# Optimization experiments

Measured on AMD Instinct MI355X. Metric: run time of the kernel, lower is better.

The kernel has to match this reference:

```python
import jax, jax.numpy as jnp
import numpy as np

N_NODES = 50000
N_EDGES = 1600000
IN_FEATS = 128
ENC_H = 20
DEC_H = 64


def setup_inputs() -> dict:
    key = jax.random.key(0)
    ks = jax.random.split(key, 14)
    inp = {}
    inp["x"] = jax.random.normal(ks[0], (N_NODES, IN_FEATS), dtype=jnp.float32)
    inp["edge_index"] = jax.random.randint(ks[1], (2, N_EDGES), 0, N_NODES, dtype=jnp.int64)
    inp["node_id"] = 0
    inp["noise_normal"] = jax.random.normal(ks[2], (N_EDGES, ENC_H), dtype=jnp.float32)
    inp["noise_u"] = jax.random.uniform(ks[3], (N_EDGES, 1), dtype=jnp.float32)
    # parameters (glorot-ish init)
    def lin(k, fan_in, fan_out):
        s = 1.0 / np.sqrt(fan_in)
        return jax.random.uniform(k, (fan_in, fan_out), jnp.float32, -s, s)
    inp["W_gc"] = lin(ks[4], IN_FEATS, ENC_H)
    inp["b_gc"] = jnp.zeros((ENC_H,), jnp.float32)
    inp["W_mu"] = lin(ks[5], 3 * ENC_H, ENC_H)
    inp["b_mu"] = jnp.zeros((ENC_H,), jnp.float32)
    inp["W_var"] = lin(ks[6], 3 * ENC_H, ENC_H)
    inp["b_var"] = jnp.zeros((ENC_H,), jnp.float32)
    inp["W_d1"] = lin(ks[7], ENC_H, DEC_H)
    inp["b_d1"] = jnp.zeros((DEC_H,), jnp.float32)
    inp["W_d2"] = lin(ks[8], DEC_H, 1)
    inp["b_d2"] = jnp.zeros((1,), jnp.float32)
    return inp


def _gcn_conv(x, edge_index, W, b):
    """PyG-style GCNConv: add self-loops, symmetric D^-1/2 (A+I) D^-1/2 norm."""
    n = x.shape[0]
    sl = jnp.arange(n, dtype=edge_index.dtype)
    row = jnp.concatenate([edge_index[0], sl])  # source
    col = jnp.concatenate([edge_index[1], sl])  # target
    xw = x @ W  # [N, H]
    deg = jax.ops.segment_sum(jnp.ones_like(col, dtype=xw.dtype), col, num_segments=n)
    dinv = jnp.where(deg > 0, jax.lax.rsqrt(deg), 0.0)
    norm = dinv[row] * dinv[col]  # [E+N]
    out = jax.ops.segment_sum(xw[row] * norm[:, None], col, num_segments=n)
    return out + b


def reference(x, edge_index, node_id, noise_normal, noise_u,
              W_gc, b_gc, W_mu, b_mu, W_var, b_var, W_d1, b_d1, W_d2, b_d2):
    # GCN encoder
    x1 = jax.nn.relu(_gcn_conv(x, edge_index, W_gc, b_gc))  # [N, H]
    # per-edge concat: [src_embed | dst_embed | node_id_embed]
    rows, cols = edge_index[0], edge_index[1]
    node_embed = jnp.broadcast_to(x1[node_id][None, :], (rows.shape[0], x1.shape[1]))
    x2 = jnp.concatenate([x1[rows], x1[cols], node_embed], axis=1)  # [E, 3H]
    # variational heads + reparameterization
    mu = x2 @ W_mu + b_mu
    sigma = jnp.exp(x2 @ W_var + b_var)
    z = mu + sigma * noise_normal  # [E, H]
    # decoder MLP
    h = jax.nn.relu(z @ W_d1 + b_d1)
    sampling_weights = jax.nn.relu(h @ W_d2 + b_d2)  # [E, 1]
    # gumbel-sigmoid sample (training=True, bias=0.0 -> bias'=1e-4, temperature=1.0)
    bias = 0.0001
    eps = (bias - (1.0 - bias)) * noise_u + (1.0 - bias)
    gate = jnp.log(eps) - jnp.log(1.0 - eps) + sampling_weights
    return jax.nn.sigmoid(gate)
```

## Files before the change

kernel.cpp:

```cpp
#include <hip/hip_runtime.h>

#define NFEAT 128
#define H 20
#define DH 64
#define SCAN_T 1024
#define BE 64
#define CAP 96

typedef __attribute__((ext_vector_type(8))) short short8;
typedef __attribute__((ext_vector_type(4))) float f32x4;

__device__ __forceinline__ unsigned short f2bf(float f) {
    union { float f; unsigned u; } v; v.f = f;
    unsigned r = v.u + 0x7fff + ((v.u >> 16) & 1);
    return (unsigned short)(r >> 16);
}
__device__ __forceinline__ unsigned pk2(unsigned short a, unsigned short b) {
    return (unsigned)a | ((unsigned)b << 16);
}

template <int CTRL>
__device__ __forceinline__ float dpp_add(float x) {
    int y = __builtin_amdgcn_update_dpp(0, __float_as_int(x), CTRL, 0xF, 0xF, true);
    return x + __int_as_float(y);
}
__device__ __forceinline__ float sum16(float x) {
    x = dpp_add<0xB1>(x);
    x = dpp_add<0x4E>(x);
    x = dpp_add<0x124>(x);
    x = dpp_add<0x128>(x);
    return x;
}

__global__ __launch_bounds__(256) void k_prep(const float* __restrict__ Wmu, const float* __restrict__ Wvar,
                                              const float* __restrict__ Wd1,
                                              const float* __restrict__ bmu, const float* __restrict__ bvar,
                                              unsigned short* __restrict__ Bh, unsigned short* __restrict__ Bd1,
                                              float* __restrict__ bcat, int* __restrict__ deg, int N) {
    int t = blockIdx.x * blockDim.x + threadIdx.x;
    if (t < N) deg[t] = 0;
    if (t < 512) {
        int f = t >> 6, l = t & 63;
        int tile = f >> 1, s = f & 1;
        int col = (tile & 1) * 16 + (l & 15);
        const float* W = (tile < 2) ? Wmu : Wvar;
#pragma unroll
        for (int j = 0; j < 8; j++) {
            int k = s * 32 + (l >> 4) * 8 + j;
            float v = (k < 3 * H && col < H) ? W[k * H + col] : 0.f;
            Bh[(size_t)f * 512 + l * 8 + j] = f2bf(v);
        }
    } else if (t < 768) {
        int f = (t - 512) >> 6, l = t & 63;
        int n = f * 16 + (l & 15);
#pragma unroll
        for (int j = 0; j < 8; j++) {
            int k = (l >> 4) * 8 + j;
            float v = (k < H) ? Wd1[k * DH + n] : 0.f;
            Bd1[(size_t)f * 512 + l * 8 + j] = f2bf(v);
        }
    } else if (t < 808) {
        int c = t - 768;
        bcat[c] = (c < H) ? bmu[c] : bvar[c - H];
    }
}

__global__ __launch_bounds__(256) void k_bucket_slots(const int* __restrict__ rows, const int* __restrict__ cols,
                                                      int* __restrict__ deg, unsigned short* __restrict__ slots, int E) {
    int e = blockIdx.x * blockDim.x + threadIdx.x;
    if (e >= E) return;
    int c = __builtin_nontemporal_load(cols + e);
    int r = __builtin_nontemporal_load(rows + e);
    int pos = atomicAdd(&deg[c], 1);
    if (pos < CAP) slots[(size_t)c * CAP + pos] = (unsigned short)r;
}

__global__ __launch_bounds__(256) void k_deg(const int* __restrict__ cols, int* __restrict__ deg, int E) {
    int t = blockIdx.x * blockDim.x + threadIdx.x;
    if (t < E) atomicAdd(&deg[cols[t]], 1);
}

__global__ __launch_bounds__(SCAN_T) void k_scan(const int* __restrict__ deg, int* __restrict__ offsets,
                                                 int* __restrict__ cursor, int N) {
    __shared__ int sums[SCAN_T];
    int t = threadIdx.x;
    int chunk = (N + SCAN_T - 1) / SCAN_T;
    int beg = t * chunk;
    int end = min(beg + chunk, N);
    int s = 0;
    for (int i = beg; i < end; i++) s += deg[i];
    sums[t] = s;
    __syncthreads();
    for (int off = 1; off < SCAN_T; off <<= 1) {
        int v = (t >= off) ? sums[t - off] : 0;
        __syncthreads();
        sums[t] += v;
        __syncthreads();
    }
    int run = (t == 0) ? 0 : sums[t - 1];
    for (int i = beg; i < end; i++) {
        offsets[i] = run;
        cursor[i] = run;
        run += deg[i];
    }
    if (t == SCAN_T - 1) offsets[N] = sums[SCAN_T - 1];
}

__global__ __launch_bounds__(256) void k_bucket_csr(const int* __restrict__ rows, const int* __restrict__ cols,
                                                    int* __restrict__ cursor, int* __restrict__ srcs, int E) {
    int e = blockIdx.x * blockDim.x + threadIdx.x;
    if (e >= E) return;
    int pos = atomicAdd(&cursor[cols[e]], 1);
    srcs[pos] = rows[e];
}

__global__ __launch_bounds__(256) void k_xw_xs(const float* __restrict__ x, const float* __restrict__ Wgc,
                                               const int* __restrict__ deg,
                                               float* __restrict__ xs, int N) {
    __shared__ float Ws[NFEAT * H];
    for (int i = threadIdx.x; i < NFEAT * H; i += blockDim.x) Ws[i] = Wgc[i];
    __syncthreads();
    int n = blockIdx.x * blockDim.x + threadIdx.x;
    if (n >= N) return;
    float acc[H];
#pragma unroll
    for (int j = 0; j < H; j++) acc[j] = 0.f;
    const float4* x4 = (const float4*)(x + (size_t)n * NFEAT);
#pragma unroll 4
    for (int k4 = 0; k4 < NFEAT / 4; k4++) {
        float4 xv = x4[k4];
#pragma unroll
        for (int s = 0; s < 4; s++) {
            float xk = (s == 0) ? xv.x : (s == 1) ? xv.y : (s == 2) ? xv.z : xv.w;
            const float4* wrow = (const float4*)(Ws + (k4 * 4 + s) * H);
#pragma unroll
            for (int q = 0; q < 5; q++) {
                float4 w = wrow[q];
                acc[q * 4 + 0] += xk * w.x;
                acc[q * 4 + 1] += xk * w.y;
                acc[q * 4 + 2] += xk * w.z;
                acc[q * 4 + 3] += xk * w.w;
            }
        }
    }
    float di = rsqrtf((float)(deg[n] + 1));
    float4* o = (float4*)(xs + (size_t)n * H);
#pragma unroll
    for (int q = 0; q < 5; q++)
        o[q] = make_float4(acc[q * 4 + 0] * di, acc[q * 4 + 1] * di, acc[q * 4 + 2] * di, acc[q * 4 + 3] * di);
}

template <typename IT>
__device__ __forceinline__ void gather_core16(const float* __restrict__ xs, const IT* __restrict__ idx,
                                              int beg, int end, int n, int sl, int degn,
                                              const float* __restrict__ bgc, unsigned short* __restrict__ x1b) {
    float acc[H];
    if (sl == 0) {
        const float4* self = (const float4*)(xs + (size_t)n * H);
#pragma unroll
        for (int q = 0; q < 5; q++) {
            float4 v = self[q];
            acc[q * 4 + 0] = v.x; acc[q * 4 + 1] = v.y; acc[q * 4 + 2] = v.z; acc[q * 4 + 3] = v.w;
        }
    } else {
#pragma unroll
        for (int j = 0; j < H; j++) acc[j] = 0.f;
    }
#pragma unroll 2
    for (int i = beg + sl; i < end; i += 16) {
        int r = (int)__builtin_nontemporal_load(idx + i);
        const float4* p = (const float4*)(xs + (size_t)r * H);
#pragma unroll
        for (int q = 0; q < 5; q++) {
            float4 v = p[q];
            acc[q * 4 + 0] += v.x; acc[q * 4 + 1] += v.y; acc[q * 4 + 2] += v.z; acc[q * 4 + 3] += v.w;
        }
    }
#pragma unroll
    for (int j = 0; j < H; j++) acc[j] = sum16(acc[j]);
    if (sl == 0) {
        float di = rsqrtf((float)(degn + 1));
        unsigned o[10];
#pragma unroll
        for (int j = 0; j < 10; j++) {
            float v0 = fmaxf(di * acc[2 * j] + bgc[2 * j], 0.f);
            float v1 = fmaxf(di * acc[2 * j + 1] + bgc[2 * j + 1], 0.f);
            o[j] = pk2(f2bf(v0), f2bf(v1));
        }
        unsigned* dst = (unsigned*)(x1b + (size_t)n * H);
        *(uint4*)dst = make_uint4(o[0], o[1], o[2], o[3]);
        *(uint4*)(dst + 4) = make_uint4(o[4], o[5], o[6], o[7]);
        *(uint2*)(dst + 8) = make_uint2(o[8], o[9]);
    }
}

__global__ __launch_bounds__(256) void k_gather_slots(const float* __restrict__ xs, const unsigned short* __restrict__ slots,
                                                      const int* __restrict__ deg, const float* __restrict__ bgc,
                                                      unsigned short* __restrict__ x1b, int N) {
    int wave = (blockIdx.x * 256 + threadIdx.x) >> 6;
    int lane = threadIdx.x & 63;
    int n = wave * 4 + (lane >> 4);
    if (n >= N) return;
    int dg = deg[n];
    int d = min(dg, CAP);
    gather_core16(xs, slots + (size_t)n * CAP, 0, d, n, lane & 15, dg, bgc, x1b);
}

__global__ __launch_bounds__(256) void k_gather_csr(const float* __restrict__ xs, const int* __restrict__ srcs,
                                                    const int* __restrict__ offsets, const int* __restrict__ deg,
                                                    const float* __restrict__ bgc,
                                                    unsigned short* __restrict__ x1b, int N) {
    int wave = (blockIdx.x * 256 + threadIdx.x) >> 6;
    int lane = threadIdx.x & 63;
    int n = wave * 4 + (lane >> 4);
    if (n >= N) return;
    gather_core16(xs, srcs, offsets[n], offsets[n + 1], n, lane & 15, deg[n], bgc, x1b);
}

__global__ __launch_bounds__(256, 8) void k_mlp(
    const unsigned short* __restrict__ x1b, const int* __restrict__ rows, const int* __restrict__ cols,
    const int* __restrict__ node_id, const float* __restrict__ noise_n, const float* __restrict__ noise_u,
    const unsigned short* __restrict__ Bh, const unsigned short* __restrict__ Bd1g,
    const float* __restrict__ bcat, const float* __restrict__ b_d1,
    const float* __restrict__ W_d2, const float* __restrict__ b_d2,
    float* __restrict__ out, int E) {

    __shared__ __align__(16) unsigned short x2s[BE * 72];
    __shared__ __align__(16) unsigned short A2[BE * 44];

    int tid = threadIdx.x;
    int e0 = blockIdx.x * BE;
    int l = tid & 63, w = tid >> 6;
    int m = l & 15, quad = l >> 4;
    int erow0 = w * 16 + quad * 4;

    float nz0[4], nz1[4];
#pragma unroll
    for (int r4 = 0; r4 < 4; r4++) {
        int e = e0 + erow0 + r4;
        int ec = (e < E) ? e : 0;
        nz0[r4] = noise_n[(size_t)ec * H + m];
        nz1[r4] = (m < 4) ? noise_n[(size_t)ec * H + 16 + m] : 0.f;
    }

    {
        int le = tid >> 2, p = tid & 3;
        int e = e0 + le; if (e >= E) e = E - 1;
        int r = rows[e], c = cols[e];
        int nid = node_id[0];
#pragma unroll
        for (int ii = 0; ii < 4; ii++) {
            int i = p + ii * 4;
            unsigned* dst = (unsigned*)((char*)x2s + le * 144 + i * 8);
            if (i < 15) {
                int node = (i < 5) ? r : (i < 10) ? c : nid;
                int cc = (i < 5) ? i : (i < 10) ? i - 5 : i - 10;
                uint2 v = *(const uint2*)((const char*)x1b + (size_t)node * 40 + cc * 8);
                dst[0] = v.x;
                dst[1] = v.y;
            } else {
                dst[0] = 0u; dst[1] = 0u;
            }
        }
    }
    __syncthreads();

    f32x4 accs[4];
    {
        const char* arow = (const char*)x2s + (w * 16 + m) * 144 + quad * 16;
        short8 a0 = *(const short8*)(arow);
        short8 a1 = *(const short8*)(arow + 64);
#pragma unroll
        for (int t4 = 0; t4 < 4; t4++) {
            f32x4 acc = {0.f, 0.f, 0.f, 0.f};
            short8 b0 = *(const short8*)(Bh + (t4 * 2 + 0) * 512 + l * 8);
            short8 b1 = *(const short8*)(Bh + (t4 * 2 + 1) * 512 + l * 8);
            acc = __builtin_amdgcn_mfma_f32_16x16x32_bf16(a0, b0, acc, 0, 0, 0);
            acc = __builtin_amdgcn_mfma_f32_16x16x32_bf16(a1, b1, acc, 0, 0, 0);
            accs[t4] = acc;
        }
    }

    {
        float bm0 = bcat[m];
        float bv0 = bcat[20 + m];
        float bm1 = (m < 4) ? bcat[16 + m] : 0.f;
        float bv1 = (m < 4) ? bcat[36 + m] : 0.f;
#pragma unroll
        for (int r4 = 0; r4 < 4; r4++) {
            float z0 = accs[0][r4] + bm0 + expf(accs[2][r4] + bv0) * nz0[r4];
            *(unsigned short*)((char*)A2 + (erow0 + r4) * 88 + m * 2) = f2bf(z0);
            unsigned short z1v = 0;
            if (m < 4) z1v = f2bf(accs[1][r4] + bm1 + expf(accs[3][r4] + bv1) * nz1[r4]);
            *(unsigned short*)((char*)A2 + (erow0 + r4) * 88 + (16 + m) * 2) = z1v;
        }
    }
    __syncthreads();

    {
        short8 a2 = *(const short8*)((const char*)A2 + (w * 16 + m) * 88 + quad * 16);
        float p0 = 0.f, p1 = 0.f, p2 = 0.f, p3 = 0.f;
#pragma unroll
        for (int t4 = 0; t4 < 4; t4++) {
            f32x4 acc = {0.f, 0.f, 0.f, 0.f};
            short8 bb = *(const short8*)(Bd1g + t4 * 512 + l * 8);
            acc = __builtin_amdgcn_mfma_f32_16x16x32_bf16(a2, bb, acc, 0, 0, 0);
            int col = t4 * 16 + m;
            float bias = b_d1[col], wo = W_d2[col];
            p0 += fmaxf(acc[0] + bias, 0.f) * wo;
            p1 += fmaxf(acc[1] + bias, 0.f) * wo;
            p2 += fmaxf(acc[2] + bias, 0.f) * wo;
            p3 += fmaxf(acc[3] + bias, 0.f) * wo;
        }
        p0 = sum16(p0); p1 = sum16(p1); p2 = sum16(p2); p3 = sum16(p3);
        if (m < 4) {
            float swv = (m == 0) ? p0 : (m == 1) ? p1 : (m == 2) ? p2 : p3;
            int leo = w * 16 + quad * 4 + m;
            int e = e0 + leo;
            if (e < E) {
                float sw = fmaxf(swv + b_d2[0], 0.f);
                float u = noise_u[e];
                float ev = 0.9999f - 0.9998f * u;
                float t = expf(-sw);
                out[e] = ev / (ev + (1.f - ev) * t);
            }
        }
    }
}

extern "C" void kernel_launch(void* const* d_in, const int* in_sizes, int n_in,
                              void* d_out, int out_size, void* d_ws, size_t ws_size,
                              hipStream_t stream) {
    const int N = in_sizes[0] / NFEAT;
    const int E = in_sizes[1] / 2;

    const float* x       = (const float*)d_in[0];
    const int*   ei      = (const int*)d_in[1];
    const int*   rows    = ei;
    const int*   cols    = ei + E;
    const int*   node_id = (const int*)d_in[2];
    const float* noise_n = (const float*)d_in[3];
    const float* noise_u = (const float*)d_in[4];
    const float* Wgc  = (const float*)d_in[5];
    const float* bgc  = (const float*)d_in[6];
    const float* Wmu  = (const float*)d_in[7];
    const float* bmu  = (const float*)d_in[8];
    const float* Wvar = (const float*)d_in[9];
    const float* bvar = (const float*)d_in[10];
    const float* Wd1  = (const float*)d_in[11];
    const float* bd1  = (const float*)d_in[12];
    const float* Wd2  = (const float*)d_in[13];
    const float* bd2  = (const float*)d_in[14];
    float* out = (float*)d_out;

    const int B = 256;
    int gN  = (N + B - 1) / B;
    int gG  = (N + 15) / 16;
    int gE  = (E + B - 1) / B;
    int gM  = (E + BE - 1) / BE;

    char* ws = (char*)d_ws;
    size_t slots_b = (size_t)N * CAP * 2;
    bool slot_path = (ws_size >= (size_t)(200000 + slots_b + 4000000 + 2000000 + 16384));

    if (slot_path) {
        int*   deg   = (int*)ws;
        unsigned short* slots = (unsigned short*)(ws + 200000);
        float* xs    = (float*)(ws + 200000 + slots_b);
        char*  p     = ws + 200000 + slots_b + 4000000;
        unsigned short* x1b = (unsigned short*)p;
        unsigned short* Bh  = (unsigned short*)(p + 2000000);
        unsigned short* Bd1 = (unsigned short*)(p + 2008192);
        float* bcat  = (float*)(p + 2012288);

        k_prep<<<gN, B, 0, stream>>>(Wmu, Wvar, Wd1, bmu, bvar, Bh, Bd1, bcat, deg, N);
        k_bucket_slots<<<gE, B, 0, stream>>>(rows, cols, deg, slots, E);
        k_xw_xs<<<gN, B, 0, stream>>>(x, Wgc, deg, xs, N);
        k_gather_slots<<<gG, B, 0, stream>>>(xs, slots, deg, bgc, x1b, N);
        k_mlp<<<gM, B, 0, stream>>>(x1b, rows, cols, node_id, noise_n, noise_u,
                                    Bh, Bd1, bcat, bd1, Wd2, bd2, out, E);
    } else {
        int*   deg     = (int*)ws;
        int*   offsets = (int*)(ws + 200000);
        int*   cursor  = (int*)(ws + 400016);
        int*   srcs    = (int*)(ws + 600016);
        float* xs      = (float*)(ws + 7000016);
        unsigned short* x1b = (unsigned short*)(ws + 11000016);
        unsigned short* Bh  = (unsigned short*)(ws + 13000016);
        unsigned short* Bd1 = (unsigned short*)(ws + 13008208);
        float* bcat    = (float*)(ws + 13012304);

        k_prep<<<gN, B, 0, stream>>>(Wmu, Wvar, Wd1, bmu, bvar, Bh, Bd1, bcat, deg, N);
        k_deg<<<gE, B, 0, stream>>>(cols, deg, E);
        k_scan<<<1, SCAN_T, 0, stream>>>(deg, offsets, cursor, N);
        k_bucket_csr<<<gE, B, 0, stream>>>(rows, cols, cursor, srcs, E);
        k_xw_xs<<<gN, B, 0, stream>>>(x, Wgc, deg, xs, N);
        k_gather_csr<<<gG, B, 0, stream>>>(xs, srcs, offsets, deg, bgc, x1b, N);
        k_mlp<<<gM, B, 0, stream>>>(x1b, rows, cols, node_id, noise_n, noise_u,
                                    Bh, Bd1, bcat, bd1, Wd2, bd2, out, E);
    }
}
```

Measured before the change: 454.9 us.

## Replace global-atomic slot bucketing with LDS-histogram deterministic CSR build

Replaces the capped per-node slot buckets, which were filled with global atomics, by a multi-pass CSR construction. Each of 128 blocks builds a byte-packed shared-memory histogram of its edge chunk. Per-node degrees, offsets and per-block deltas are then derived with small scans, and a placement pass writes 16-bit sources into a compact CSR. This removes contended global atomics and the padded slot array; the CAP truncation goes away, so high-degree nodes are handled correctly. In exchange it adds several kernel launches and extra passes over cols and the histogram. The 8-bit per-block counters could overflow if one node gets more than 255 edges within a single chunk.

```diff
diff --git a/kernel.cpp b/kernel.cpp
--- a/kernel.cpp
+++ b/kernel.cpp
@@ -5,7 +5,8 @@
 #define DH 64
 #define SCAN_T 1024
 #define BE 64
-#define CAP 96
+#define NB 128
+#define HW 12800
 
 typedef __attribute__((ext_vector_type(8))) short short8;
 typedef __attribute__((ext_vector_type(4))) float f32x4;
@@ -65,14 +66,115 @@
     }
 }
 
-__global__ __launch_bounds__(256) void k_bucket_slots(const int* __restrict__ rows, const int* __restrict__ cols,
-                                                      int* __restrict__ deg, unsigned short* __restrict__ slots, int E) {
-    int e = blockIdx.x * blockDim.x + threadIdx.x;
-    if (e >= E) return;
-    int c = __builtin_nontemporal_load(cols + e);
-    int r = __builtin_nontemporal_load(rows + e);
-    int pos = atomicAdd(&deg[c], 1);
-    if (pos < CAP) slots[(size_t)c * CAP + pos] = (unsigned short)r;
+
+__global__ __launch_bounds__(512) void k_hist(const int* __restrict__ cols,
+                                              unsigned* __restrict__ hist, int E, int N) {
+    __shared__ unsigned h[HW];
+    int wstride = (N + 3) >> 2;
+    for (int i = threadIdx.x; i < wstride; i += 512) h[i] = 0;
+    __syncthreads();
+    int chunk = (E + NB - 1) / NB;
+    int beg = blockIdx.x * chunk, end = min(beg + chunk, E);
+    for (int i = beg + threadIdx.x; i < end; i += 512) {
+        int c = __builtin_nontemporal_load(cols + i);
+        atomicAdd(&h[c >> 2], 1u << ((c & 3) * 8));
+    }
+    __syncthreads();
+    unsigned* dst = hist + (size_t)blockIdx.x * wstride;
+    for (int i = threadIdx.x; i < wstride; i += 512) dst[i] = h[i];
+}
+
+__global__ __launch_bounds__(256) void k_sumbins(const unsigned* __restrict__ hist,
+                                                 int* __restrict__ deg, int* __restrict__ chunkSum, int N) {
+    __shared__ int sc[256];
+    int c = blockIdx.x * 256 + threadIdx.x;
+    int wstride = (N + 3) >> 2;
+    int sh = (c & 3) * 8;
+    int d = 0;
+    if (c < N) {
+#pragma unroll 4
+        for (int b = 0; b < NB; b++) d += (hist[(size_t)b * wstride + (c >> 2)] >> sh) & 0xFF;
+        deg[c] = d;
+    }
+    sc[threadIdx.x] = d;
+    __syncthreads();
+    for (int off = 128; off > 0; off >>= 1) {
+        if (threadIdx.x < off) sc[threadIdx.x] += sc[threadIdx.x + off];
+        __syncthreads();
+    }
+    if (threadIdx.x == 0) chunkSum[blockIdx.x] = sc[0];
+}
+
+__global__ __launch_bounds__(256) void k_scansmall(const int* __restrict__ chunkSum,
+                                                   int* __restrict__ chunkOff, int nb) {
+    __shared__ int sc[256];
+    int t = threadIdx.x;
+    int v0 = (t < nb) ? chunkSum[t] : 0;
+    sc[t] = v0;
+    __syncthreads();
+    for (int off = 1; off < 256; off <<= 1) {
+        int v = (t >= off) ? sc[t - off] : 0;
+        __syncthreads();
+        sc[t] += v;
+        __syncthreads();
+    }
+    if (t < nb) chunkOff[t] = sc[t] - v0;
+}
+
+__global__ __launch_bounds__(256) void k_bases(const unsigned* __restrict__ hist,
+                                               const int* __restrict__ chunkOff,
+                                               unsigned char* __restrict__ delta,
+                                               int* __restrict__ offsets, int N, int E) {
+    __shared__ int sc[256];
+    int c = blockIdx.x * 256 + threadIdx.x;
+    int wstride = (N + 3) >> 2;
+    int sh = (c & 3) * 8;
+    int d = 0;
+    if (c < N) {
+#pragma unroll 4
+        for (int b = 0; b < NB; b++) d += (hist[(size_t)b * wstride + (c >> 2)] >> sh) & 0xFF;
+    }
+    sc[threadIdx.x] = d;
+    __syncthreads();
+    for (int off = 1; off < 256; off <<= 1) {
+        int v = (threadIdx.x >= off) ? sc[threadIdx.x - off] : 0;
+        __syncthreads();
+        sc[threadIdx.x] += v;
+        __syncthreads();
+    }
+    if (c < N) {
+        int base = chunkOff[blockIdx.x] + sc[threadIdx.x] - d;
+        offsets[c] = base;
+        int run = 0;
+#pragma unroll 4
+        for (int b = 0; b < NB; b++) {
+            delta[(size_t)b * N + c] = (unsigned char)run;
+            run += (hist[(size_t)b * wstride + (c >> 2)] >> sh) & 0xFF;
+        }
+    }
+    if (blockIdx.x == 0 && threadIdx.x == 0) offsets[N] = E;
+}
+
+__global__ __launch_bounds__(512) void k_place(const int* __restrict__ rows, const int* __restrict__ cols,
+                                               const int* __restrict__ offsets,
+                                               const unsigned char* __restrict__ delta,
+                                               unsigned short* __restrict__ srcs, int E, int N) {
+    __shared__ unsigned h[HW];
+    int wstride = (N + 3) >> 2;
+    for (int i = threadIdx.x; i < wstride; i += 512) h[i] = 0;
+    __syncthreads();
+    int chunk = (E + NB - 1) / NB;
+    int beg = blockIdx.x * chunk, end = min(beg + chunk, E);
+    const unsigned char* mydelta = delta + (size_t)blockIdx.x * N;
+    for (int i = beg + threadIdx.x; i < end; i += 512) {
+        int c = __builtin_nontemporal_load(cols + i);
+        int r = __builtin_nontemporal_load(rows + i);
+        int sh = (c & 3) * 8;
+        unsigned old = atomicAdd(&h[c >> 2], 1u << sh);
+        int rank = (old >> sh) & 0xFF;
+        int pos = offsets[c] + (int)mydelta[c] + rank;
+        srcs[pos] = (unsigned short)r;
+    }
 }
 
 __global__ __launch_bounds__(256) void k_deg(const int* __restrict__ cols, int* __restrict__ deg, int E) {
@@ -194,16 +296,15 @@
     }
 }
 
-__global__ __launch_bounds__(256) void k_gather_slots(const float* __restrict__ xs, const unsigned short* __restrict__ slots,
-                                                      const int* __restrict__ deg, const float* __restrict__ bgc,
+__global__ __launch_bounds__(256) void k_gather_csr16(const float* __restrict__ xs, const unsigned short* __restrict__ srcs,
+                                                      const int* __restrict__ offsets, const int* __restrict__ deg,
+                                                      const float* __restrict__ bgc,
                                                       unsigned short* __restrict__ x1b, int N) {
     int wave = (blockIdx.x * 256 + threadIdx.x) >> 6;
     int lane = threadIdx.x & 63;
     int n = wave * 4 + (lane >> 4);
     if (n >= N) return;
-    int dg = deg[n];
-    int d = min(dg, CAP);
-    gather_core16(xs, slots + (size_t)n * CAP, 0, d, n, lane & 15, dg, bgc, x1b);
+    gather_core16(xs, srcs, offsets[n], offsets[n + 1], n, lane & 15, deg[n], bgc, x1b);
 }
 
 __global__ __launch_bounds__(256) void k_gather_csr(const float* __restrict__ xs, const int* __restrict__ srcs,
@@ -358,25 +459,48 @@
     int gG  = (N + 15) / 16;
     int gE  = (E + B - 1) / B;
     int gM  = (E + BE - 1) / BE;
+    int nBins = (N + 255) / 256;
 
     char* ws = (char*)d_ws;
-    size_t slots_b = (size_t)N * CAP * 2;
-    bool slot_path = (ws_size >= (size_t)(200000 + slots_b + 4000000 + 2000000 + 16384));
-
-    if (slot_path) {
-        int*   deg   = (int*)ws;
-        unsigned short* slots = (unsigned short*)(ws + 200000);
-        float* xs    = (float*)(ws + 200000 + slots_b);
-        char*  p     = ws + 200000 + slots_b + 4000000;
-        unsigned short* x1b = (unsigned short*)p;
-        unsigned short* Bh  = (unsigned short*)(p + 2000000);
-        unsigned short* Bd1 = (unsigned short*)(p + 2008192);
-        float* bcat  = (float*)(p + 2012288);
+    size_t o_deg     = 0;
+    size_t o_off     = o_deg  + (((size_t)N * 4 + 255) & ~255ULL);
+    size_t o_csum    = o_off  + (((size_t)(N + 1) * 4 + 255) & ~255ULL);
+    size_t o_coff    = o_csum + 1024;
+    size_t o_hist    = o_coff + 1024;
+    size_t wstride   = (size_t)((N + 3) >> 2);
+    size_t o_delta   = o_hist  + ((NB * wstride * 4 + 255) & ~255ULL);
+    size_t o_srcs    = o_delta + (((size_t)NB * N + 255) & ~255ULL);
+    size_t o_xs      = o_srcs  + (((size_t)E * 2 + 255) & ~255ULL);
+    size_t o_x1b     = o_xs    + (((size_t)N * H * 4 + 255) & ~255ULL);
+    size_t o_Bh      = o_x1b   + (((size_t)N * H * 2 + 255) & ~255ULL);
+    size_t o_Bd1     = o_Bh    + 8192;
+    size_t o_bcat    = o_Bd1   + 4096;
+    size_t need      = o_bcat  + 256;
+
+    bool main_path = (ws_size >= need) && (N <= 4 * HW) && (N < 65536) && (nBins <= 256);
+
+    if (main_path) {
+        int*   deg     = (int*)(ws + o_deg);
+        int*   offsets = (int*)(ws + o_off);
+        int*   csum    = (int*)(ws + o_csum);
+        int*   coff    = (int*)(ws + o_coff);
+        unsigned* hist = (unsigned*)(ws + o_hist);
+        unsigned char* delta = (unsigned char*)(ws + o_delta);
+        unsigned short* srcs = (unsigned short*)(ws + o_srcs);
+        float* xs      = (float*)(ws + o_xs);
+        unsigned short* x1b  = (unsigned short*)(ws + o_x1b);
+        unsigned short* Bh   = (unsigned short*)(ws + o_Bh);
+        unsigned short* Bd1  = (unsigned short*)(ws + o_Bd1);
+        float* bcat    = (float*)(ws + o_bcat);
 
         k_prep<<<gN, B, 0, stream>>>(Wmu, Wvar, Wd1, bmu, bvar, Bh, Bd1, bcat, deg, N);
-        k_bucket_slots<<<gE, B, 0, stream>>>(rows, cols, deg, slots, E);
+        k_hist<<<NB, 512, 0, stream>>>(cols, hist, E, N);
+        k_sumbins<<<nBins, B, 0, stream>>>(hist, deg, csum, N);
+        k_scansmall<<<1, B, 0, stream>>>(csum, coff, nBins);
+        k_bases<<<nBins, B, 0, stream>>>(hist, coff, delta, offsets, N, E);
         k_xw_xs<<<gN, B, 0, stream>>>(x, Wgc, deg, xs, N);
-        k_gather_slots<<<gG, B, 0, stream>>>(xs, slots, deg, bgc, x1b, N);
+        k_place<<<NB, 512, 0, stream>>>(rows, cols, offsets, delta, srcs, E, N);
+        k_gather_csr16<<<gG, B, 0, stream>>>(xs, srcs, offsets, deg, bgc, x1b, N);
         k_mlp<<<gM, B, 0, stream>>>(x1b, rows, cols, node_id, noise_n, noise_u,
                                     Bh, Bd1, bcat, bd1, Wd2, bd2, out, E);
     } else {
```

New measurement: 448.2 us. No clear change (-1.5%).
